# Performance work log

Measured on AMD Instinct MI355X. Metric: run time of the kernel, lower is better.

## Reference

```python
import jax, jax.numpy as jnp
import numpy as np

SHRINK_THRES = 0.0025
EPS = 1e-12


def setup_inputs() -> dict:
    key = jax.random.key(0)
    k1, k2 = jax.random.split(key)
    N, C, H, W = 32, 256, 32, 32
    M = 2000
    x = jax.random.normal(k1, (N, C, H, W), dtype=jnp.float32)
    # torch init: uniform(-stdv, stdv), stdv = 1/sqrt(fea_dim)
    stdv = 1.0 / np.sqrt(C)
    weight = jax.random.uniform(k2, (M, C), dtype=jnp.float32, minval=-stdv, maxval=stdv)
    return {"x": x, "weight": weight}


def hard_shrink_relu(a, lambd=SHRINK_THRES, epsilon=EPS):
    d = a - lambd
    return jax.nn.relu(d) * a / (jnp.abs(d) + epsilon)


def reference(x, weight):
    N, C, H, W = x.shape
    M = weight.shape[0]
    # N x C x H x W -> (N*H*W) x C
    xt = jnp.transpose(x, (0, 2, 3, 1)).reshape(-1, C)  # (T, C)
    att = xt @ weight.T                                  # (T, M)
    att = jax.nn.softmax(att, axis=1)
    att = hard_shrink_relu(att)
    # L1 normalize over memory dim (torch F.normalize p=1, eps=1e-12)
    att = att / jnp.maximum(jnp.sum(jnp.abs(att), axis=1, keepdims=True), 1e-12)
    y = att @ weight                                     # (T, C)
    y = y.reshape(N, H, W, C).transpose(0, 3, 1, 2)      # N x C x H x W
    att = att.reshape(N, H, W, M).transpose(0, 3, 1, 2)  # N x M x H x W
    return (y, att)
```

## Files before the change

kernel.cpp:

```cpp
#include <hip/hip_runtime.h>

typedef _Float16 f16x8 __attribute__((ext_vector_type(8)));
typedef float    f32x4 __attribute__((ext_vector_type(4)));

constexpr int Nn = 32, Cc = 256, HW = 1024, Mm = 2000, Tt = 32768;
constexpr int TB = 64;
constexpr int XROW = 264;
constexpr int YROW = 257;
constexpr int LCAP = 768;
constexpr int NT = 32;
constexpr float LAMBDA = 0.0025f;
constexpr float PLO = LAMBDA * (1.0f - 3e-3f);
constexpr float PHI = LAMBDA * (1.0f + 3e-3f);
constexpr float ECUT = 4.8f;
constexpr float SCL = 4096.0f, ISCL = 1.0f / 4096.0f;

__global__ void wcvt_kernel(const float* __restrict__ w,
                            _Float16* __restrict__ whi, _Float16* __restrict__ wlo) {
  int i = blockIdx.x * 256 + threadIdx.x;
  if (i < Mm * Cc) {
    float v = w[i];
    _Float16 h = (_Float16)v;
    whi[i] = h;
    wlo[i] = (_Float16)((v - (float)h) * SCL);
  }
}

__device__ __forceinline__ void gl_lds16(const void* g, void* l) {
  __builtin_amdgcn_global_load_lds(
      (const __attribute__((address_space(1))) void*)g,
      (__attribute__((address_space(3))) void*)l, 16, 0, 0);
}

__global__ __launch_bounds__(512, 2)
void fused_mem_kernel(const float* __restrict__ x, const float* __restrict__ wgt,
                      const _Float16* __restrict__ whi, const _Float16* __restrict__ wlo,
                      float* __restrict__ y_out, float* __restrict__ att_out) {
  __shared__ __align__(16) float bufB[32768];
  __shared__ int   lm[LCAP];
  __shared__ float le[LCAP];
  __shared__ float la[LCAP];
  __shared__ float Zred[256];
  __shared__ float invZ[TB];
  __shared__ float l1s[TB];
  __shared__ float dens[TB];
  __shared__ int   lcnt;
  _Float16* Xh = (_Float16*)bufB;
  _Float16* Xl = Xh + TB * XROW;
  float*    yL = bufB;
  char*     Bb = (char*)bufB;

  const int tid = threadIdx.x;
  const int wv  = tid >> 6;
  const int l   = tid & 63;
  const int qw  = l >> 4;
  const int lr  = l & 15;
  const int mh  = wv & 3;
  const int tp  = wv >> 2;
  const int t0  = blockIdx.x * TB;
  const int n   = t0 >> 10;
  const int hw0 = t0 & 1023;

  if (tid == 0) lcnt = 0;
  if (tid < TB) l1s[tid] = 0.f;

  {
    const int h = tid & 63, cb = tid >> 6;
    const float* xp = x + ((size_t)n * Cc) * HW + hw0 + h;
    #pragma unroll
    for (int j = 0; j < 32; ++j) {
      int c = cb * 32 + j;
      float v = xp[(size_t)c * HW];
      _Float16 hh = (_Float16)v;
      Xh[h * XROW + c] = hh;
      Xl[h * XROW + c] = (_Float16)((v - (float)hh) * SCL);
    }
  }
  __syncthreads();

  f16x8 a0h[8], a0l[8], a1h[8], a1l[8];
  #pragma unroll
  for (int ks = 0; ks < 8; ++ks) {
    const int r0 = (tp * 32 + lr) * XROW + ks * 32 + qw * 8;
    const int r1 = (tp * 32 + 16 + lr) * XROW + ks * 32 + qw * 8;
    a0h[ks] = *(const f16x8*)&Xh[r0];
    a0l[ks] = *(const f16x8*)&Xl[r0];
    a1h[ks] = *(const f16x8*)&Xh[r1];
    a1l[ks] = *(const f16x8*)&Xl[r1];
  }
  __syncthreads();

  auto stage = [&](int b, int tile) {
    char* base = Bb + b * 65536;
    #pragma unroll
    for (int i = 0; i < 8; ++i) {
      const int bu = i * 512 + wv * 64;
      const int u2 = bu + l;
      const int r64 = (u2 >> 5) & 63;
      const int chunk = u2 & 31;
      int mrow = tile * 64 + r64; mrow = mrow < Mm ? mrow : (Mm - 1);
      const char* src = (const char*)(u2 < 2048 ? whi : wlo)
                      + (size_t)mrow * 512 + ((chunk ^ (r64 & 7)) << 4);
      gl_lds16(src, base + u2 * 16);
    }
  };

  stage(0, 0);
  __syncthreads();

  float zp0[4] = {0.f, 0.f, 0.f, 0.f};
  float zp1[4] = {0.f, 0.f, 0.f, 0.f};
  const int rrow = mh * 16 + lr;
  const int rsw  = rrow & 7;
  int cur = 0;
  for (int t = 0; t < NT; ++t) {
    if (t + 1 < NT) stage(cur ^ 1, t + 1);

    #pragma unroll
    for (int jj = 0; jj < 2; ++jj) {
      int m = t * 64 + jj * 32 + (tid >> 4);
      if (m < Mm) {
        f32x4 z4 = {0.f, 0.f, 0.f, 0.f};
        *(f32x4*)(att_out + ((size_t)(n * Mm + m)) * HW + hw0 + ((tid & 15) << 2)) = z4;
      }
    }

    if (t < NT - 1 || mh == 0) {
      const char* bb = Bb + cur * 65536;
      f32x4 ahh0 = {0.f,0.f,0.f,0.f}, axl0 = {0.f,0.f,0.f,0.f}, alh0 = {0.f,0.f,0.f,0.f};
      f32x4 ahh1 = {0.f,0.f,0.f,0.f}, axl1 = {0.f,0.f,0.f,0.f}, alh1 = {0.f,0.f,0.f,0.f};
      #pragma unroll
      for (int kc = 0; kc < 2; ++kc) {
        f16x8 bh[4], bl[4];
        #pragma unroll
        for (int k4 = 0; k4 < 4; ++k4) {
          const int ks = kc * 4 + k4;
          const int ch = rrow * 512 + (((ks * 4 + qw) ^ rsw) << 4);
          bh[k4] = *(const f16x8*)(bb + ch);
          bl[k4] = *(const f16x8*)(bb + 32768 + ch);
        }
        #pragma unroll
        for (int k4 = 0; k4 < 4; ++k4) {
          const int ks = kc * 4 + k4;
          ahh0 = __builtin_amdgcn_mfma_f32_16x16x32_f16(a0h[ks], bh[k4], ahh0, 0, 0, 0);
          axl0 = __builtin_amdgcn_mfma_f32_16x16x32_f16(a0h[ks], bl[k4], axl0, 0, 0, 0);
          alh0 = __builtin_amdgcn_mfma_f32_16x16x32_f16(a0l[ks], bh[k4], alh0, 0, 0, 0);
          ahh1 = __builtin_amdgcn_mfma_f32_16x16x32_f16(a1h[ks], bh[k4], ahh1, 0, 0, 0);
          axl1 = __builtin_amdgcn_mfma_f32_16x16x32_f16(a1h[ks], bl[k4], axl1, 0, 0, 0);
          alh1 = __builtin_amdgcn_mfma_f32_16x16x32_f16(a1l[ks], bh[k4], alh1, 0, 0, 0);
        }
      }
      const int mrow_ = t * 64 + rrow;
      #pragma unroll
      for (int r = 0; r < 4; ++r) {
        float s0 = fmaf(axl0[r] + alh0[r], ISCL, ahh0[r]);
        float e0 = __expf(s0);
        zp0[r] += e0;
        if (e0 > ECUT) {
          int slot = atomicAdd(&lcnt, 1);
          if (slot < LCAP) { lm[slot] = ((tp * 32 + qw * 4 + r) << 16) | mrow_; le[slot] = e0; }
        }
        float s1 = fmaf(axl1[r] + alh1[r], ISCL, ahh1[r]);
        float e1 = __expf(s1);
        zp1[r] += e1;
        if (e1 > ECUT) {
          int slot = atomicAdd(&lcnt, 1);
          if (slot < LCAP) { lm[slot] = ((tp * 32 + 16 + qw * 4 + r) << 16) | mrow_; le[slot] = e1; }
        }
      }
    }
    __syncthreads();
    cur ^= 1;
  }

  #pragma unroll
  for (int o = 1; o < 16; o <<= 1)
    #pragma unroll
    for (int r = 0; r < 4; ++r) {
      zp0[r] += __shfl_xor(zp0[r], o);
      zp1[r] += __shfl_xor(zp1[r], o);
    }
  if (lr == 0) {
    #pragma unroll
    for (int r = 0; r < 4; ++r) {
      Zred[mh * 64 + tp * 32 + qw * 4 + r]      = zp0[r];
      Zred[mh * 64 + tp * 32 + 16 + qw * 4 + r] = zp1[r];
    }
  }
  __syncthreads();

  if (tid < TB)
    invZ[tid] = 1.f / (Zred[tid] + Zred[64 + tid] + Zred[128 + tid] + Zred[192 + tid]);
  __syncthreads();

  const int ne = min(lcnt, LCAP);
  for (int e = tid; e < ne; e += 512) {
    const int tm = lm[e];
    const int t = tm >> 16, m = tm & 0xFFFF;
    float p = le[e] * invZ[t];
    float a = 0.f;
    if (p > PLO) {
      float pu = p;
      if (p < PHI) {
        const float* xr = x + ((size_t)n * Cc) * HW + hw0 + t;
        const float* wr = wgt + (size_t)m * Cc;
        float s = 0.f;
        for (int c = 0; c < Cc; ++c) s = fmaf(xr[(size_t)c * HW], wr[c], s);
        pu = expf(s) * invZ[t];
      }
      float d = pu - LAMBDA;
      if (d > 0.f) {
        a = (d * pu) / (d + 1e-12f);
        atomicAdd(&l1s[t], a);
      }
    }
    la[e] = a;
  }
  __syncthreads();

  if (tid < TB) dens[tid] = fmaxf(l1s[tid], 1e-12f);
  for (int i = tid; i < TB * YROW; i += 512) yL[i] = 0.f;
  __syncthreads();

  for (int e = wv; e < ne; e += 8) {
    float av = la[e];
    if (av > 0.f) {
      const int tm = lm[e];
      const int t = tm >> 16, m = tm & 0xFFFF;
      const float a = av / dens[t];
      float4 wf = *(const float4*)(wgt + (size_t)m * Cc + l * 4);
      float* yr = yL + t * YROW + l;
      atomicAdd(yr + 0,   a * wf.x);
      atomicAdd(yr + 64,  a * wf.y);
      atomicAdd(yr + 128, a * wf.z);
      atomicAdd(yr + 192, a * wf.w);
      if (l == 0)
        att_out[((size_t)(n * Mm + m)) * HW + hw0 + t] = a;
    }
  }
  __syncthreads();

  {
    const int h = tid & 63, cb = tid >> 6;
    float* yp = y_out + ((size_t)n * Cc) * HW + hw0 + h;
    #pragma unroll
    for (int j = 0; j < 32; ++j) {
      int c = cb * 32 + j;
      yp[(size_t)c * HW] = yL[h * YROW + (((c & 3) << 6) | (c >> 2))];
    }
  }
}

extern "C" void kernel_launch(void* const* d_in, const int* in_sizes, int n_in,
                              void* d_out, int out_size, void* d_ws, size_t ws_size,
                              hipStream_t stream) {
  const float* x = (const float*)d_in[0];
  const float* w = (const float*)d_in[1];
  float* y_out   = (float*)d_out;
  float* att_out = y_out + (size_t)Nn * Cc * HW;
  _Float16* whi = (_Float16*)d_ws;
  _Float16* wlo = whi + (size_t)Mm * Cc;

  wcvt_kernel<<<(Mm * Cc + 255) / 256, 256, 0, stream>>>(w, whi, wlo);
  fused_mem_kernel<<<Tt / TB, 512, 0, stream>>>(x, w, whi, wlo, y_out, att_out);
}
```

Before: 588.4 us.

## Stage weight tiles through registers instead of direct global-to-LDS loads

```diff
diff --git a/kernel.cpp b/kernel.cpp
--- a/kernel.cpp
+++ b/kernel.cpp
@@ -24,12 +24,6 @@
     whi[i] = h;
     wlo[i] = (_Float16)((v - (float)h) * SCL);
   }
-}
-
-__device__ __forceinline__ void gl_lds16(const void* g, void* l) {
-  __builtin_amdgcn_global_load_lds(
-      (const __attribute__((address_space(1))) void*)g,
-      (__attribute__((address_space(3))) void*)l, 16, 0, 0);
 }
 
 __global__ __launch_bounds__(512, 2)
@@ -90,23 +84,33 @@
   }
   __syncthreads();
 
-  auto stage = [&](int b, int tile) {
-    char* base = Bb + b * 65536;
+  float4 rs[8];
+  auto ldW = [&](int tile) {
     #pragma unroll
     for (int i = 0; i < 8; ++i) {
-      const int bu = i * 512 + wv * 64;
-      const int u2 = bu + l;
+      const int u2 = i * 512 + wv * 64 + l;
       const int r64 = (u2 >> 5) & 63;
       const int chunk = u2 & 31;
       int mrow = tile * 64 + r64; mrow = mrow < Mm ? mrow : (Mm - 1);
-      const char* src = (const char*)(u2 < 2048 ? whi : wlo)
+      const char* src = (const char*)(i < 4 ? whi : wlo)
                       + (size_t)mrow * 512 + ((chunk ^ (r64 & 7)) << 4);
-      gl_lds16(src, base + u2 * 16);
+      rs[i] = *(const float4*)src;
     }
   };
-
-  stage(0, 0);
-  __syncthreads();
+  auto wrW = [&](int b) {
+    char* base = Bb + b * 65536;
+    #pragma unroll
+    for (int i = 0; i < 8; ++i) {
+      const int u2 = i * 512 + wv * 64 + l;
+      *(float4*)(base + u2 * 16) = rs[i];
+    }
+  };
+
+  ldW(0);
+  wrW(0);
+  ldW(1);
+  asm volatile("s_waitcnt lgkmcnt(0)" ::: "memory");
+  __builtin_amdgcn_s_barrier();
 
   float zp0[4] = {0.f, 0.f, 0.f, 0.f};
   float zp1[4] = {0.f, 0.f, 0.f, 0.f};
@@ -114,8 +118,6 @@
   const int rsw  = rrow & 7;
   int cur = 0;
   for (int t = 0; t < NT; ++t) {
-    if (t + 1 < NT) stage(cur ^ 1, t + 1);
-
     #pragma unroll
     for (int jj = 0; jj < 2; ++jj) {
       int m = t * 64 + jj * 32 + (tid >> 4);
@@ -169,7 +171,12 @@
         }
       }
     }
-    __syncthreads();
+
+    __builtin_amdgcn_sched_barrier(0);
+    if (t + 1 < NT) wrW(cur ^ 1);
+    if (t + 2 < NT) ldW(t + 2);
+    asm volatile("s_waitcnt lgkmcnt(0)" ::: "memory");
+    __builtin_amdgcn_s_barrier();
     cur ^= 1;
   }
 
```

Result: slower. 813.7 us (+38.3%).

## Drop LDS weight staging, read fp16 weights directly from global with smaller blocks

Applied to the files above, without the earlier changes.

```diff
diff --git a/kernel.cpp b/kernel.cpp
--- a/kernel.cpp
+++ b/kernel.cpp
@@ -4,11 +4,12 @@
 typedef float    f32x4 __attribute__((ext_vector_type(4)));
 
 constexpr int Nn = 32, Cc = 256, HW = 1024, Mm = 2000, Tt = 32768;
-constexpr int TB = 64;
+constexpr int TB = 32;
 constexpr int XROW = 264;
 constexpr int YROW = 257;
-constexpr int LCAP = 768;
+constexpr int LCAP = 448;
 constexpr int NT = 32;
+constexpr int BUFN = TB * YROW;
 constexpr float LAMBDA = 0.0025f;
 constexpr float PLO = LAMBDA * (1.0f - 3e-3f);
 constexpr float PHI = LAMBDA * (1.0f + 3e-3f);
@@ -26,37 +27,28 @@
   }
 }
 
-__device__ __forceinline__ void gl_lds16(const void* g, void* l) {
-  __builtin_amdgcn_global_load_lds(
-      (const __attribute__((address_space(1))) void*)g,
-      (__attribute__((address_space(3))) void*)l, 16, 0, 0);
-}
-
-__global__ __launch_bounds__(512, 2)
+__global__ __launch_bounds__(256, 2)
 void fused_mem_kernel(const float* __restrict__ x, const float* __restrict__ wgt,
                       const _Float16* __restrict__ whi, const _Float16* __restrict__ wlo,
                       float* __restrict__ y_out, float* __restrict__ att_out) {
-  __shared__ __align__(16) float bufB[32768];
+  __shared__ __align__(16) float bufB[BUFN];
   __shared__ int   lm[LCAP];
   __shared__ float le[LCAP];
   __shared__ float la[LCAP];
-  __shared__ float Zred[256];
+  __shared__ float Zred[128];
   __shared__ float invZ[TB];
   __shared__ float l1s[TB];
   __shared__ float dens[TB];
   __shared__ int   lcnt;
-  _Float16* Xh = (_Float16*)bufB;
-  _Float16* Xl = Xh + TB * XROW;
+  _Float16* Xs = (_Float16*)bufB;
   float*    yL = bufB;
-  char*     Bb = (char*)bufB;
 
   const int tid = threadIdx.x;
   const int wv  = tid >> 6;
   const int l   = tid & 63;
   const int qw  = l >> 4;
   const int lr  = l & 15;
-  const int mh  = wv & 3;
-  const int tp  = wv >> 2;
+  const int mh  = wv;
   const int t0  = blockIdx.x * TB;
   const int n   = t0 >> 10;
   const int hw0 = t0 & 1023;
@@ -64,69 +56,59 @@
   if (tid == 0) lcnt = 0;
   if (tid < TB) l1s[tid] = 0.f;
 
+  f16x8 a0h[8], a0l[8], a1h[8], a1l[8];
   {
-    const int h = tid & 63, cb = tid >> 6;
+    const int h = tid & 31, cb = tid >> 5;
+    const float* xp = x + ((size_t)n * Cc) * HW + hw0 + h;
+    #pragma unroll
+    for (int j = 0; j < 32; ++j) {
+      int c = cb * 32 + j;
+      float v = xp[(size_t)c * HW];
+      Xs[h * XROW + c] = (_Float16)v;
+    }
+  }
+  __syncthreads();
+  #pragma unroll
+  for (int ks = 0; ks < 8; ++ks) {
+    a0h[ks] = *(const f16x8*)&Xs[lr * XROW + ks * 32 + qw * 8];
+    a1h[ks] = *(const f16x8*)&Xs[(16 + lr) * XROW + ks * 32 + qw * 8];
+  }
+  __syncthreads();
+  {
+    const int h = tid & 31, cb = tid >> 5;
     const float* xp = x + ((size_t)n * Cc) * HW + hw0 + h;
     #pragma unroll
     for (int j = 0; j < 32; ++j) {
       int c = cb * 32 + j;
       float v = xp[(size_t)c * HW];
       _Float16 hh = (_Float16)v;
-      Xh[h * XROW + c] = hh;
-      Xl[h * XROW + c] = (_Float16)((v - (float)hh) * SCL);
-    }
-  }
-  __syncthreads();
-
-  f16x8 a0h[8], a0l[8], a1h[8], a1l[8];
+      Xs[h * XROW + c] = (_Float16)((v - (float)hh) * SCL);
+    }
+  }
+  __syncthreads();
   #pragma unroll
   for (int ks = 0; ks < 8; ++ks) {
-    const int r0 = (tp * 32 + lr) * XROW + ks * 32 + qw * 8;
-    const int r1 = (tp * 32 + 16 + lr) * XROW + ks * 32 + qw * 8;
-    a0h[ks] = *(const f16x8*)&Xh[r0];
-    a0l[ks] = *(const f16x8*)&Xl[r0];
-    a1h[ks] = *(const f16x8*)&Xh[r1];
-    a1l[ks] = *(const f16x8*)&Xl[r1];
-  }
-  __syncthreads();
-
-  auto stage = [&](int b, int tile) {
-    char* base = Bb + b * 65536;
-    #pragma unroll
-    for (int i = 0; i < 8; ++i) {
-      const int bu = i * 512 + wv * 64;
-      const int u2 = bu + l;
-      const int r64 = (u2 >> 5) & 63;
-      const int chunk = u2 & 31;
-      int mrow = tile * 64 + r64; mrow = mrow < Mm ? mrow : (Mm - 1);
-      const char* src = (const char*)(u2 < 2048 ? whi : wlo)
-                      + (size_t)mrow * 512 + ((chunk ^ (r64 & 7)) << 4);
-      gl_lds16(src, base + u2 * 16);
-    }
-  };
-
-  stage(0, 0);
+    a0l[ks] = *(const f16x8*)&Xs[lr * XROW + ks * 32 + qw * 8];
+    a1l[ks] = *(const f16x8*)&Xs[(16 + lr) * XROW + ks * 32 + qw * 8];
+  }
   __syncthreads();
 
   float zp0[4] = {0.f, 0.f, 0.f, 0.f};
   float zp1[4] = {0.f, 0.f, 0.f, 0.f};
   const int rrow = mh * 16 + lr;
-  const int rsw  = rrow & 7;
-  int cur = 0;
+
   for (int t = 0; t < NT; ++t) {
-    if (t + 1 < NT) stage(cur ^ 1, t + 1);
-
     #pragma unroll
     for (int jj = 0; jj < 2; ++jj) {
-      int m = t * 64 + jj * 32 + (tid >> 4);
+      int m = t * 64 + jj * 32 + (tid >> 3);
       if (m < Mm) {
         f32x4 z4 = {0.f, 0.f, 0.f, 0.f};
-        *(f32x4*)(att_out + ((size_t)(n * Mm + m)) * HW + hw0 + ((tid & 15) << 2)) = z4;
+        *(f32x4*)(att_out + ((size_t)(n * Mm + m)) * HW + hw0 + ((tid & 7) << 2)) = z4;
       }
     }
 
     if (t < NT - 1 || mh == 0) {
-      const char* bb = Bb + cur * 65536;
+      const size_t rb = (size_t)(t * 64 + rrow) * Cc + qw * 8;
       f32x4 ahh0 = {0.f,0.f,0.f,0.f}, axl0 = {0.f,0.f,0.f,0.f}, alh0 = {0.f,0.f,0.f,0.f};
       f32x4 ahh1 = {0.f,0.f,0.f,0.f}, axl1 = {0.f,0.f,0.f,0.f}, alh1 = {0.f,0.f,0.f,0.f};
       #pragma unroll
@@ -135,19 +117,17 @@
         #pragma unroll
         for (int k4 = 0; k4 < 4; ++k4) {
           const int ks = kc * 4 + k4;
-          const int ch = rrow * 512 + (((ks * 4 + qw) ^ rsw) << 4);
-          bh[k4] = *(const f16x8*)(bb + ch);
-          bl[k4] = *(const f16x8*)(bb + 32768 + ch);
+          bh[k4] = *(const f16x8*)(whi + rb + ks * 32);
+          bl[k4] = *(const f16x8*)(wlo + rb + ks * 32);
         }
         #pragma unroll
         for (int k4 = 0; k4 < 4; ++k4) {
-          const int ks = kc * 4 + k4;
-          ahh0 = __builtin_amdgcn_mfma_f32_16x16x32_f16(a0h[ks], bh[k4], ahh0, 0, 0, 0);
-          axl0 = __builtin_amdgcn_mfma_f32_16x16x32_f16(a0h[ks], bl[k4], axl0, 0, 0, 0);
-          alh0 = __builtin_amdgcn_mfma_f32_16x16x32_f16(a0l[ks], bh[k4], alh0, 0, 0, 0);
-          ahh1 = __builtin_amdgcn_mfma_f32_16x16x32_f16(a1h[ks], bh[k4], ahh1, 0, 0, 0);
-          axl1 = __builtin_amdgcn_mfma_f32_16x16x32_f16(a1h[ks], bl[k4], axl1, 0, 0, 0);
-          alh1 = __builtin_amdgcn_mfma_f32_16x16x32_f16(a1l[ks], bh[k4], alh1, 0, 0, 0);
+          ahh0 = __builtin_amdgcn_mfma_f32_16x16x32_f16(a0h[kc*4+k4], bh[k4], ahh0, 0, 0, 0);
+          axl0 = __builtin_amdgcn_mfma_f32_16x16x32_f16(a0h[kc*4+k4], bl[k4], axl0, 0, 0, 0);
+          alh0 = __builtin_amdgcn_mfma_f32_16x16x32_f16(a0l[kc*4+k4], bh[k4], alh0, 0, 0, 0);
+          ahh1 = __builtin_amdgcn_mfma_f32_16x16x32_f16(a1h[kc*4+k4], bh[k4], ahh1, 0, 0, 0);
+          axl1 = __builtin_amdgcn_mfma_f32_16x16x32_f16(a1h[kc*4+k4], bl[k4], axl1, 0, 0, 0);
+          alh1 = __builtin_amdgcn_mfma_f32_16x16x32_f16(a1l[kc*4+k4], bh[k4], alh1, 0, 0, 0);
         }
       }
       const int mrow_ = t * 64 + rrow;
@@ -158,19 +138,17 @@
         zp0[r] += e0;
         if (e0 > ECUT) {
           int slot = atomicAdd(&lcnt, 1);
-          if (slot < LCAP) { lm[slot] = ((tp * 32 + qw * 4 + r) << 16) | mrow_; le[slot] = e0; }
+          if (slot < LCAP) { lm[slot] = ((qw * 4 + r) << 16) | mrow_; le[slot] = e0; }
         }
         float s1 = fmaf(axl1[r] + alh1[r], ISCL, ahh1[r]);
         float e1 = __expf(s1);
         zp1[r] += e1;
         if (e1 > ECUT) {
           int slot = atomicAdd(&lcnt, 1);
-          if (slot < LCAP) { lm[slot] = ((tp * 32 + 16 + qw * 4 + r) << 16) | mrow_; le[slot] = e1; }
-        }
-      }
-    }
-    __syncthreads();
-    cur ^= 1;
+          if (slot < LCAP) { lm[slot] = ((16 + qw * 4 + r) << 16) | mrow_; le[slot] = e1; }
+        }
+      }
+    }
   }
 
   #pragma unroll
@@ -183,18 +161,18 @@
   if (lr == 0) {
     #pragma unroll
     for (int r = 0; r < 4; ++r) {
-      Zred[mh * 64 + tp * 32 + qw * 4 + r]      = zp0[r];
-      Zred[mh * 64 + tp * 32 + 16 + qw * 4 + r] = zp1[r];
+      Zred[mh * 32 + qw * 4 + r]      = zp0[r];
+      Zred[mh * 32 + 16 + qw * 4 + r] = zp1[r];
     }
   }
   __syncthreads();
 
   if (tid < TB)
-    invZ[tid] = 1.f / (Zred[tid] + Zred[64 + tid] + Zred[128 + tid] + Zred[192 + tid]);
+    invZ[tid] = 1.f / (Zred[tid] + Zred[32 + tid] + Zred[64 + tid] + Zred[96 + tid]);
   __syncthreads();
 
   const int ne = min(lcnt, LCAP);
-  for (int e = tid; e < ne; e += 512) {
+  for (int e = tid; e < ne; e += 256) {
     const int tm = lm[e];
     const int t = tm >> 16, m = tm & 0xFFFF;
     float p = le[e] * invZ[t];
@@ -219,10 +197,10 @@
   __syncthreads();
 
   if (tid < TB) dens[tid] = fmaxf(l1s[tid], 1e-12f);
-  for (int i = tid; i < TB * YROW; i += 512) yL[i] = 0.f;
-  __syncthreads();
-
-  for (int e = wv; e < ne; e += 8) {
+  for (int i = tid; i < BUFN; i += 256) yL[i] = 0.f;
+  __syncthreads();
+
+  for (int e = wv; e < ne; e += 4) {
     float av = la[e];
     if (av > 0.f) {
       const int tm = lm[e];
@@ -241,7 +219,7 @@
   __syncthreads();
 
   {
-    const int h = tid & 63, cb = tid >> 6;
+    const int h = tid & 31, cb = tid >> 5;
     float* yp = y_out + ((size_t)n * Cc) * HW + hw0 + h;
     #pragma unroll
     for (int j = 0; j < 32; ++j) {
@@ -262,5 +240,5 @@
   _Float16* wlo = whi + (size_t)Mm * Cc;
 
   wcvt_kernel<<<(Mm * Cc + 255) / 256, 256, 0, stream>>>(w, whi, wlo);
-  fused_mem_kernel<<<Tt / TB, 512, 0, stream>>>(x, w, whi, wlo, y_out, att_out);
+  fused_mem_kernel<<<Tt / TB, 256, 0, stream>>>(x, w, whi, wlo, y_out, att_out);
 }
```

Measured after the change: 649.0 us. 1.1x slower.
